# Performance work log

Measured on AMD Instinct MI355X. Metric: run time of the kernel, lower is better.

The kernel has to match this reference:

```python
import jax, jax.numpy as jnp
from jax import lax
import numpy as np

COMMITMENT_COST = 0.25
DATA_VARIANCE = 1.0
DN = ('NCHW', 'OIHW', 'NCHW')


def _conv(x, w, b, stride, pad):
    y = lax.conv_general_dilated(x, w, (stride, stride), ((pad, pad), (pad, pad)), dimension_numbers=DN)
    return y + b[None, :, None, None]


def _conv_t(x, w, b, stride, pad, out_pad):
    # PyTorch ConvTranspose2d(w: [Cin, Cout, kH, kW]) == dilated conv with flipped, transposed kernel
    wf = jnp.flip(w, (2, 3)).transpose(1, 0, 2, 3)  # -> [Cout, Cin, kH, kW]
    k = w.shape[2]
    lo, hi = k - 1 - pad, k - 1 - pad + out_pad
    y = lax.conv_general_dilated(x, wf, (1, 1), ((lo, hi), (lo, hi)), lhs_dilation=(stride, stride), dimension_numbers=DN)
    return y + b[None, :, None, None]


def setup_inputs() -> dict:
    key = jax.random.key(0)
    ks = jax.random.split(key, 14)
    n = lambda k, shp, s: (jax.random.normal(k, shp, dtype=jnp.float32) * s)
    return {
        'x': n(ks[0], (64, 3, 256, 256), 1.0),
        'enc_w1': n(ks[1], (32, 3, 3, 3), 0.2), 'enc_b1': n(ks[2], (32,), 0.02),
        'enc_w2': n(ks[3], (64, 32, 3, 3), 0.06), 'enc_b2': n(ks[4], (64,), 0.02),
        'enc_w3': n(ks[5], (16, 64, 1, 1), 0.12), 'enc_b3': n(ks[6], (16,), 0.02),
        'codebook': n(ks[7], (512, 16), 1.0),
        'dec_w1': n(ks[8], (16, 64, 3, 3), 0.08), 'dec_b1': n(ks[9], (64,), 0.02),
        'dec_w2': n(ks[10], (64, 32, 3, 3), 0.04), 'dec_b2': n(ks[11], (32,), 0.02),
        'dec_w3': n(ks[12], (32, 3, 3, 3), 0.06), 'dec_b3': n(ks[13], (3,), 0.02),
    }


def reference(x, enc_w1, enc_b1, enc_w2, enc_b2, enc_w3, enc_b3, codebook,
              dec_w1, dec_b1, dec_w2, dec_b2, dec_w3, dec_b3):
    # Encoder: 3 -> 32 (s2) -> 64 (s2) -> D (1x1)
    z = jax.nn.relu(_conv(x, enc_w1, enc_b1, 2, 1))
    z = jax.nn.relu(_conv(z, enc_w2, enc_b2, 2, 1))
    z = _conv(z, enc_w3, enc_b3, 1, 0)  # [B, D, H/4, W/4]

    # Vector quantization (training path)
    zp = z.transpose(0, 2, 3, 1)                      # [B, h, w, D]
    D = zp.shape[-1]
    flat = zp.reshape(-1, D)                          # [N, D]
    dist = (jnp.sum(flat * flat, axis=1, keepdims=True)
            + jnp.sum(codebook * codebook, axis=1)
            - 2.0 * flat @ codebook.T)                # [N, K]
    idx = jnp.argmin(dist, axis=1)                    # [N]
    quantized = codebook[idx].reshape(zp.shape)       # [B, h, w, D]

    q_latent_loss = jnp.mean((quantized - lax.stop_gradient(zp)) ** 2)
    e_latent_loss = jnp.mean((zp - lax.stop_gradient(quantized)) ** 2)
    e_q_loss = q_latent_loss + COMMITMENT_COST * e_latent_loss

    ste = zp + lax.stop_gradient(quantized - zp)      # straight-through
    e = ste.transpose(0, 3, 1, 2)                     # [B, D, h, w]

    # Decoder: D -> 64 (x2) -> 32 (x2) -> 3
    y = jax.nn.relu(_conv_t(e, dec_w1, dec_b1, 2, 1, 1))
    y = jax.nn.relu(_conv_t(y, dec_w2, dec_b2, 2, 1, 1))
    x_recon = _conv_t(y, dec_w3, dec_b3, 1, 1, 0)

    recon_mse = jnp.mean((x_recon - x) ** 2)
    recon_loss = recon_mse / DATA_VARIANCE
    return jnp.stack([e_q_loss, recon_loss, recon_mse])
```

## Files before the change

kernel.cpp:

```cpp
#include <hip/hip_runtime.h>
#include <hip/hip_bf16.h>


typedef __attribute__((ext_vector_type(8))) short bf16x8;
typedef __attribute__((ext_vector_type(4))) float f32x4;
typedef unsigned short ushort_t;

__device__ __forceinline__ ushort_t f2bf(float v) {
    __hip_bfloat16 h = __float2bfloat16(v);
    return *(ushort_t*)&h;
}
__device__ __forceinline__ float bf2f(ushort_t u) {
    __hip_bfloat16 h = *(__hip_bfloat16*)&u;
    return __bfloat162float(h);
}
__device__ __forceinline__ unsigned pack2r(float a, float b) {
    return (unsigned)f2bf(fmaxf(a, 0.f)) | ((unsigned)f2bf(fmaxf(b, 0.f)) << 16);
}


__global__ void zero_k(float* __restrict__ acc) {
    acc[blockIdx.x * 256 + threadIdx.x] = 0.f;
}

__global__ __launch_bounds__(256) void prep_k(
        const float* __restrict__ ew1, const float* __restrict__ ew2,
        const float* __restrict__ dw1, const float* __restrict__ dw2,
        const float* __restrict__ dw3, const float* __restrict__ cb,
        ushort_t* __restrict__ wt, float* __restrict__ cn) {
    int idx = blockIdx.x * 256 + threadIdx.x;
    if (idx < 1024) {
        int co = idx >> 5, k = idx & 31;
        wt[idx] = (k < 27) ? f2bf(ew1[co * 27 + k]) : (ushort_t)0;
    } else if (idx < 19456) {
        int i = idx - 1024;
        int t = i >> 11, co = (i >> 5) & 63, ci = i & 31;
        int lci = ((ci & 1) << 4) | (ci >> 1);
        wt[idx] = f2bf(ew2[co * 288 + lci * 9 + t]);
    } else if (idx < 37888) {
        int i = idx - 19456;
        int t = i >> 11, co = (i >> 5) & 63, k = i & 31;
        wt[idx] = (k < 16) ? f2bf(dw1[k * 576 + co * 9 + t]) : (ushort_t)0;
    } else if (idx < 56320) {
        int i = idx - 37888;
        int t = i >> 11, kc = (i >> 10) & 1, co = (i >> 5) & 31, ci = i & 31;
        int m = kc * 32 + ci;
        int lci = ((m & 3) << 4) | (m >> 2);
        wt[idx] = f2bf(dw2[lci * 288 + co * 9 + t]);
    } else if (idx < 60928) {
        int i = idx - 56320;
        int t = i >> 9, co = (i >> 5) & 15, ci = i & 31;
        int lci = ((ci & 1) << 4) | (ci >> 1);
        wt[idx] = (co < 3) ? f2bf(dw3[lci * 27 + co * 9 + (8 - t)]) : (ushort_t)0;
    } else if (idx < 61440) {
        int k = idx - 60928;
        float s = 0.f;
        #pragma unroll
        for (int d = 0; d < 16; ++d) { float v = cb[k * 16 + d]; s += v * v; }
        cn[k] = s;
    }
}

__global__ __launch_bounds__(256) void pad_k(ushort_t* __restrict__ d1p) {
    const int img = blockIdx.x, tid = threadIdx.x;
    const uint4 z = (uint4){0, 0, 0, 0};
    uint4* b1 = (uint4*)(d1p + (size_t)img * 1065024);
    for (int i = tid; i < 1032; i += 256) b1[132096 + i] = z;
    for (int i = tid; i < 1024; i += 256) {
        int r = i >> 3, u = i & 7;
        b1[(r * 129 + 128) * 8 + u] = z;
    }
}

__global__ __launch_bounds__(256, 4) void conv1_k(const float* __restrict__ x,
        const ushort_t* __restrict__ wt, const float* __restrict__ bias,
        ushort_t* __restrict__ a1) {
    const int by = blockIdx.y, b = by >> 7, oh = by & 127;
    const int tid = threadIdx.x;
    __shared__ __align__(16) ushort_t sX[9 * 264];
    __shared__ int sOff[32];
    for (int i = tid; i < 9 * 264 / 2; i += 256) ((unsigned*)sX)[i] = 0u;
    if (tid < 32) {
        int k = tid, off = 0;
        if (k < 27) { int ci = k / 9, r9 = k % 9, kh = r9 / 3, kw = r9 % 3;
                      off = (ci * 3 + kh) * 264 + kw; }
        sOff[tid] = off;
    }
    __syncthreads();
    #pragma unroll
    for (int it = 0; it < 9; ++it) {
        int slot = it * 256 + tid;
        int ci = slot / 768, r = slot % 768, kh = r >> 8, iw = r & 255;
        int ih = 2 * oh + kh - 1;
        float v = ((unsigned)ih < 256u) ? x[(long)(b * 3 + ci) * 65536 + ih * 256 + iw] : 0.f;
        sX[(ci * 3 + kh) * 264 + iw + 1] = f2bf(v);
    }
    __syncthreads();
    const int lane = tid & 63, wave = tid >> 6, q = lane >> 4, n16 = lane & 15;
    bf16x8 Bw[2];
    #pragma unroll
    for (int u = 0; u < 2; ++u)
        Bw[u] = *(const bf16x8*)(wt + (u * 16 + n16) * 32 + q * 8);
    f32x4 acc[2][2];
    #pragma unroll
    for (int u = 0; u < 2; ++u) {
        float bz = bias[u * 16 + n16];
        acc[0][u] = (f32x4){bz, bz, bz, bz};
        acc[1][u] = (f32x4){bz, bz, bz, bz};
    }
    #pragma unroll
    for (int mf = 0; mf < 2; ++mf) {
        const int m2 = 2 * (wave * 32 + mf * 16 + n16);
        ushort_t av[8];
        #pragma unroll
        for (int j = 0; j < 8; ++j) {
            int k = q * 8 + j;
            av[j] = (k < 27) ? sX[sOff[k] + m2] : (ushort_t)0;
        }
        bf16x8 A = *(bf16x8*)av;
        #pragma unroll
        for (int u = 0; u < 2; ++u)
            acc[mf][u] = __builtin_amdgcn_mfma_f32_16x16x32_bf16(A, Bw[u], acc[mf][u], 0, 0, 0);
    }
    #pragma unroll
    for (int mf = 0; mf < 2; ++mf)
        #pragma unroll
        for (int r = 0; r < 4; ++r) {
            int ow = wave * 32 + mf * 16 + q * 4 + r;
            *(unsigned*)(a1 + ((long)(b * 128 + oh) * 128 + ow) * 32 + n16 * 2) =
                pack2r(acc[mf][0][r], acc[mf][1][r]);
        }
}

__global__ __launch_bounds__(256, 4) void conv2_k(const ushort_t* __restrict__ a1,
        const ushort_t* __restrict__ wt, const float* __restrict__ bias,
        ushort_t* __restrict__ a2) {
    const int by = blockIdx.y, b = by >> 6, oh = by & 63;
    const int tid = threadIdx.x;
    __shared__ __align__(16) ushort_t sA[3 * 2 * 66 * 40];
    uint4* z4 = (uint4*)sA;
    #pragma unroll
    for (int it = 0; it < 8; ++it) {
        int slot = it * 256 + tid;
        if (slot < 1980) z4[slot] = (uint4){0, 0, 0, 0};
    }
    __syncthreads();
    #pragma unroll
    for (int it = 0; it < 6; ++it) {
        int slot = it * 256 + tid;
        if (slot < 1536) {
            int kh = slot >> 9, rem = slot & 511, iw = rem >> 2, ci8 = (rem & 3) << 3;
            int ih = 2 * oh + kh - 1;
            if ((unsigned)ih < 128u) {
                uint4 v = *(const uint4*)(a1 + ((long)(b * 128 + ih) * 128 + iw) * 32 + ci8);
                int idx = iw + 2, p = idx & 1, c = idx >> 1;
                *(uint4*)&sA[((kh * 2 + p) * 66 + c) * 40 + ci8] = v;
            }
        }
    }
    __syncthreads();
    const int lane = tid & 63, wave = tid >> 6, q = lane >> 4, n16 = lane & 15;
    f32x4 acc[4];
    #pragma unroll
    for (int u = 0; u < 4; ++u) {
        float bz = bias[u * 16 + n16];
        acc[u] = (f32x4){bz, bz, bz, bz};
    }
    const int ow = wave * 16 + n16;
    #pragma unroll
    for (int t = 0; t < 9; ++t) {
        const int kh = t / 3, kw = t % 3;
        const int p = (kw == 1) ? 0 : 1;
        const int c = (kw == 0) ? ow : ow + 1;
        bf16x8 A = *(bf16x8*)&sA[((kh * 2 + p) * 66 + c) * 40 + q * 8];
        #pragma unroll
        for (int u = 0; u < 4; ++u) {
            bf16x8 B = *(const bf16x8*)(wt + 1024 + t * 2048 + (u * 16 + n16) * 32 + q * 8);
            acc[u] = __builtin_amdgcn_mfma_f32_16x16x32_bf16(A, B, acc[u], 0, 0, 0);
        }
    }
    #pragma unroll
    for (int r = 0; r < 4; ++r) {
        int owo = wave * 16 + q * 4 + r;
        uint2 pk;
        pk.x = pack2r(acc[0][r], acc[1][r]);
        pk.y = pack2r(acc[2][r], acc[3][r]);
        *(uint2*)(a2 + ((long)(b * 64 + oh) * 64 + owo) * 64 + n16 * 4) = pk;
    }
}

__global__ __launch_bounds__(256) void conv3_vq_k(const ushort_t* __restrict__ a2,
        const float* __restrict__ w3, const float* __restrict__ b3,
        const float* __restrict__ cb, const float* __restrict__ cn,
        ushort_t* __restrict__ e, float* __restrict__ acc) {
    const int base = blockIdx.x * 512 + threadIdx.x;
    __shared__ float sred[4];
    float z[2][16];
    #pragma unroll
    for (int p = 0; p < 2; ++p)
        #pragma unroll
        for (int d = 0; d < 16; ++d) z[p][d] = b3[d];
    #pragma unroll
    for (int p = 0; p < 2; ++p) {
        const ushort_t* arow = a2 + (long)(base + p * 256) * 64;
        #pragma unroll
        for (int c8 = 0; c8 < 8; ++c8) {
            uint4 raw = *(const uint4*)(arow + c8 * 8);
            ushort_t us[8];
            *(uint4*)us = raw;
            #pragma unroll
            for (int j = 0; j < 8; ++j) {
                int m = c8 * 8 + j;
                int lci = ((m & 3) << 4) | (m >> 2);
                float a = bf2f(us[j]);
                #pragma unroll
                for (int d = 0; d < 16; ++d)
                    z[p][d] = fmaf(a, w3[d * 64 + lci], z[p][d]);
            }
        }
    }
    const float4* cb4 = (const float4*)cb;
    float best0 = 1e30f, best1 = 1e30f; int bi0 = 0, bi1 = 0;
    for (int k = 0; k < 512; ++k) {
        float4 c0 = cb4[k * 4 + 0], c1 = cb4[k * 4 + 1];
        float4 c2 = cb4[k * 4 + 2], c3 = cb4[k * 4 + 3];
        float nk = cn[k];
        float d0 = z[0][0]*c0.x + z[0][1]*c0.y + z[0][2]*c0.z + z[0][3]*c0.w
                 + z[0][4]*c1.x + z[0][5]*c1.y + z[0][6]*c1.z + z[0][7]*c1.w
                 + z[0][8]*c2.x + z[0][9]*c2.y + z[0][10]*c2.z + z[0][11]*c2.w
                 + z[0][12]*c3.x + z[0][13]*c3.y + z[0][14]*c3.z + z[0][15]*c3.w;
        float d1 = z[1][0]*c0.x + z[1][1]*c0.y + z[1][2]*c0.z + z[1][3]*c0.w
                 + z[1][4]*c1.x + z[1][5]*c1.y + z[1][6]*c1.z + z[1][7]*c1.w
                 + z[1][8]*c2.x + z[1][9]*c2.y + z[1][10]*c2.z + z[1][11]*c2.w
                 + z[1][12]*c3.x + z[1][13]*c3.y + z[1][14]*c3.z + z[1][15]*c3.w;
        float dist0 = nk - 2.f * d0, dist1 = nk - 2.f * d1;
        if (dist0 < best0) { best0 = dist0; bi0 = k; }
        if (dist1 < best1) { best1 = dist1; bi1 = k; }
    }
    float lsum = 0.f;
    #pragma unroll
    for (int d = 0; d < 16; ++d) {
        float q0 = cb[bi0 * 16 + d], q1 = cb[bi1 * 16 + d];
        float f0 = q0 - z[0][d], f1 = q1 - z[1][d];
        lsum += f0 * f0 + f1 * f1;
        e[(long)base * 16 + d] = f2bf(q0);
        e[(long)(base + 256) * 16 + d] = f2bf(q1);
    }
    #pragma unroll
    for (int off = 32; off > 0; off >>= 1) lsum += __shfl_down(lsum, off, 64);
    if ((threadIdx.x & 63) == 0) sred[threadIdx.x >> 6] = lsum;
    __syncthreads();
    if (threadIdx.x == 0)
        atomicAdd(&acc[(blockIdx.x & 63) << 5],
                  sred[0] + sred[1] + sred[2] + sred[3]);
}

__global__ __launch_bounds__(256, 4) void dec1_k(const ushort_t* __restrict__ e,
        const ushort_t* __restrict__ wt, const float* __restrict__ bias,
        ushort_t* __restrict__ d1p) {
    const int by = blockIdx.y, b = by >> 6, i = by & 63;
    const int tid = threadIdx.x;
    __shared__ __align__(16) ushort_t sE[2 * 66 * 24];
    uint4* z4 = (uint4*)sE;
    #pragma unroll
    for (int it = 0; it < 2; ++it) {
        int slot = it * 256 + tid;
        if (slot < 396) z4[slot] = (uint4){0, 0, 0, 0};
    }
    __syncthreads();
    {
        int dh = tid >> 7, rem = tid & 127, j = rem >> 1, ci8 = (rem & 1) * 8;
        if (i + dh < 64) {
            uint4 v = *(const uint4*)(e + ((long)((b * 64 + i + dh) * 64 + j)) * 16 + ci8);
            *(uint4*)&sE[(dh * 66 + j) * 24 + ci8] = v;
        }
    }
    __syncthreads();
    const int lane = tid & 63, wave = tid >> 6, q = lane >> 4, n16 = lane & 15;
    f32x4 acc[4][4];
    #pragma unroll
    for (int u = 0; u < 4; ++u) {
        float bz = bias[u * 16 + n16];
        #pragma unroll
        for (int c = 0; c < 4; ++c) acc[c][u] = (f32x4){bz, bz, bz, bz};
    }
    const int jl = wave * 16 + n16;
    #pragma unroll
    for (int t = 0; t < 9; ++t) {
        const int kh = t / 3, kw = t % 3;
        const int dh = (kh == 0) ? 1 : 0, dw = (kw == 0) ? 1 : 0;
        const int cls = ((kh != 1) ? 2 : 0) | ((kw != 1) ? 1 : 0);
        bf16x8 A = *(bf16x8*)&sE[(dh * 66 + jl + dw) * 24 + (q & 1) * 8];
        #pragma unroll
        for (int u = 0; u < 4; ++u) {
            bf16x8 B = *(const bf16x8*)(wt + 19456 + t * 2048 + (u * 16 + n16) * 32 + q * 8);
            acc[cls][u] = __builtin_amdgcn_mfma_f32_16x16x32_bf16(A, B, acc[cls][u], 0, 0, 0);
        }
    }
    #pragma unroll
    for (int ph = 0; ph < 2; ++ph)
        #pragma unroll
        for (int pw = 0; pw < 2; ++pw)
            #pragma unroll
            for (int r = 0; r < 4; ++r) {
                int oh = 2 * i + ph;
                int ow = 2 * (wave * 16 + q * 4 + r) + pw;
                uint2 pk;
                pk.x = pack2r(acc[ph * 2 + pw][0][r], acc[ph * 2 + pw][1][r]);
                pk.y = pack2r(acc[ph * 2 + pw][2][r], acc[ph * 2 + pw][3][r]);
                *(uint2*)(d1p + (size_t)b * 1065024 + ((long)oh * 129 + ow) * 64 + n16 * 4) = pk;
            }
}

__global__ __launch_bounds__(256, 3) void dec23_k(const ushort_t* __restrict__ d1p,
        const ushort_t* __restrict__ wt, const float* __restrict__ db2,
        const float* __restrict__ db3, const float* __restrict__ x,
        float* __restrict__ acc) {
    const int bx = blockIdx.x, by = blockIdx.y;
    const int b = by >> 6, i4 = by & 63;
    const int j0 = bx << 7;
    const int tid = threadIdx.x;
    const int lane = tid & 63, wave = tid >> 6, q = lane >> 4, n16 = lane & 15;

    __shared__ __align__(16) ushort_t sT[6 * 132 * 32];
    __shared__ float sred[4];
    uint4* z4 = (uint4*)sT;
    #pragma unroll
    for (int it = 0; it < 13; ++it) {
        int s = it * 256 + tid;
        if (s < 3168) z4[s] = (uint4){0, 0, 0, 0};
    }
    __syncthreads();

    const int bb0 = (j0 >> 1) - 1;
    const ushort_t* dbase = d1p + (size_t)b * 1065024;
    for (int s = 0; s < 3; ++s) {
        const int aidx = (wave + s) & 3;
        const int a = 2 * i4 + aidx - 1;
        const int bt0 = s * 2;
        f32x4 acc2[4][2][2];
        #pragma unroll
        for (int u = 0; u < 2; ++u) {
            float bz = db2[u * 16 + n16];
            #pragma unroll
            for (int c = 0; c < 4; ++c) {
                acc2[c][u][0] = (f32x4){bz, bz, bz, bz};
                acc2[c][u][1] = (f32x4){bz, bz, bz, bz};
            }
        }
        const bool skip0 = (aidx == 0);
        const bool skip1 = (aidx == 3);
        #pragma unroll
        for (int kc = 0; kc < 2; ++kc) {
            bf16x8 A[2][2][2];
            #pragma unroll
            for (int dh = 0; dh < 2; ++dh) {
                int row = a + dh;
                bool rok = (unsigned)row <= 128u;
                int rowc = rok ? row : 0;
                #pragma unroll
                for (int dw = 0; dw < 2; ++dw) {
                    #pragma unroll
                    for (int c = 0; c < 2; ++c) {
                        int col = bb0 + (bt0 + c) * 16 + n16 + dw;
                        bool cok = (unsigned)col <= 128u;
                        int colc = cok ? col : 0;
                        bf16x8 v = *(const bf16x8*)(dbase + ((long)rowc * 129 + colc) * 64 + kc * 32 + q * 8);
                        if (!(rok && cok)) v = (bf16x8){0, 0, 0, 0, 0, 0, 0, 0};
                        A[dh][dw][c] = v;
                    }
                }
            }
#define MF23(cls, kh, kw, dh, dw)                                                   \
            _Pragma("unroll")                                                       \
            for (int u = 0; u < 2; ++u) {                                           \
                bf16x8 Bf = *(const bf16x8*)(wt + 37888 + ((kh) * 3 + (kw)) * 2048  \
                                 + kc * 1024 + (u * 16 + n16) * 32 + q * 8);        \
                acc2[cls][u][0] = __builtin_amdgcn_mfma_f32_16x16x32_bf16(          \
                    A[dh][dw][0], Bf, acc2[cls][u][0], 0, 0, 0);                    \
                acc2[cls][u][1] = __builtin_amdgcn_mfma_f32_16x16x32_bf16(          \
                    A[dh][dw][1], Bf, acc2[cls][u][1], 0, 0, 0);                    \
            }
            if (!skip0) {
                MF23(0, 1, 1, 0, 0)
                MF23(1, 1, 0, 0, 1)  MF23(1, 1, 2, 0, 0)
            }
            if (!skip1) {
                MF23(2, 0, 1, 1, 0)  MF23(2, 2, 1, 0, 0)
                MF23(3, 0, 0, 1, 1)  MF23(3, 0, 2, 1, 0)  MF23(3, 2, 0, 0, 1)  MF23(3, 2, 2, 0, 0)
            }
#undef MF23
        }
        #pragma unroll
        for (int cls = 0; cls < 4; ++cls) {
            int ph = cls >> 1, pw = cls & 1;
            if ((ph == 0 && skip0) || (ph == 1 && skip1)) continue;
            int R = 2 * a + ph;
            if ((unsigned)R >= 256u) continue;
            int Rp = R - 4 * i4 + 1;
            #pragma unroll
            for (int c = 0; c < 2; ++c) {
                #pragma unroll
                for (int r = 0; r < 4; ++r) {
                    int cg = 2 * (bb0 + (bt0 + c) * 16 + q * 4 + r) + pw;
                    int cp = 2 * ((bt0 + c) * 16 + q * 4 + r) + pw - 1;
                    if ((unsigned)cg < 256u && (unsigned)cp < 130u) {
                        *(unsigned*)&sT[Rp * 4224 + cp * 32 + n16 * 2] =
                            pack2r(acc2[cls][0][c][r], acc2[cls][1][c][r]);
                    }
                }
            }
        }
    }
    __syncthreads();

    bf16x8 Bw[9];
    #pragma unroll
    for (int t = 0; t < 9; ++t)
        Bw[t] = *(const bf16x8*)(wt + 56320 + t * 512 + n16 * 32 + q * 8);
    float bz3 = (n16 < 3) ? db3[n16] : 0.f;
    f32x4 a4[8];
    #pragma unroll
    for (int mf = 0; mf < 8; ++mf) a4[mf] = (f32x4){bz3, bz3, bz3, bz3};
    const int oh = 4 * i4 + wave;
    #pragma unroll
    for (int kh = 0; kh < 3; ++kh) {
        const ushort_t* srow = &sT[(wave + kh) * 4224];
        #pragma unroll
        for (int mf = 0; mf < 8; ++mf) {
            #pragma unroll
            for (int kw = 0; kw < 3; ++kw) {
                bf16x8 A = *(const bf16x8*)(srow + (mf * 16 + n16 + kw) * 32 + q * 8);
                a4[mf] = __builtin_amdgcn_mfma_f32_16x16x32_bf16(A, Bw[kh * 3 + kw], a4[mf], 0, 0, 0);
            }
        }
    }
    float lsum = 0.f;
    if (n16 < 3) {
        const float* xrow = x + ((long)(b * 3 + n16) * 256 + oh) * 256 + j0;
        #pragma unroll
        for (int mf = 0; mf < 8; ++mf)
            #pragma unroll
            for (int r = 0; r < 4; ++r) {
                int ow = mf * 16 + q * 4 + r;
                float df = a4[mf][r] - xrow[ow];
                lsum += df * df;
            }
    }
    #pragma unroll
    for (int off = 32; off > 0; off >>= 1) lsum += __shfl_down(lsum, off, 64);
    if (lane == 0) sred[wave] = lsum;
    __syncthreads();
    if (tid == 0)
        atomicAdd(&acc[2048 + ((by & 63) << 5)],
                  sred[0] + sred[1] + sred[2] + sred[3]);
}

__global__ void finalize_k(const float* __restrict__ acc, float* __restrict__ out) {
    int t = threadIdx.x;
    float v = acc[t << 5];
    float m = acc[2048 + (t << 5)];
    #pragma unroll
    for (int off = 32; off > 0; off >>= 1) {
        v += __shfl_down(v, off, 64);
        m += __shfl_down(m, off, 64);
    }
    if (t == 0) {
        float eq  = 1.25f * v / 4194304.f;
        float mse = m / 12582912.f;
        out[0] = eq;
        out[1] = mse;
        out[2] = mse;
    }
}

extern "C" void kernel_launch(void* const* d_in, const int* in_sizes, int n_in,
                              void* d_out, int out_size, void* d_ws, size_t ws_size,
                              hipStream_t stream) {
    (void)in_sizes; (void)n_in; (void)out_size;
    const float* x   = (const float*)d_in[0];
    const float* ew1 = (const float*)d_in[1];
    const float* eb1 = (const float*)d_in[2];
    const float* ew2 = (const float*)d_in[3];
    const float* eb2 = (const float*)d_in[4];
    const float* ew3 = (const float*)d_in[5];
    const float* eb3 = (const float*)d_in[6];
    const float* cb  = (const float*)d_in[7];
    const float* dw1 = (const float*)d_in[8];
    const float* db1 = (const float*)d_in[9];
    const float* dw2 = (const float*)d_in[10];
    const float* db2 = (const float*)d_in[11];
    const float* dw3 = (const float*)d_in[12];
    const float* db3 = (const float*)d_in[13];
    float* out = (float*)d_out;

    int C = 64;
    while (C > 1 && (size_t)147456 + (size_t)C * 2261120UL > ws_size) C >>= 1;

    char* base = (char*)d_ws;
    float*    acc = (float*)base;
    ushort_t* wt  = (ushort_t*)(base + 16384);
    float*    cn  = (float*)(base + 16384 + 121856);
    ushort_t* e   = (ushort_t*)(base + 147456);
    char*     rgn = base + 147456 + (size_t)C * 131072UL;
    ushort_t* a1  = (ushort_t*)rgn;
    ushort_t* a2  = (ushort_t*)(rgn + (size_t)C * 1048576UL);
    ushort_t* d1p = (ushort_t*)rgn;

    zero_k<<<16, 256, 0, stream>>>(acc);
    prep_k<<<240, 256, 0, stream>>>(ew1, ew2, dw1, dw2, dw3, cb, wt, cn);

    for (int b0 = 0; b0 < 64; b0 += C) {
        const float* xc = x + (size_t)b0 * 196608UL;
        conv1_k   <<<dim3(1, C * 128), 256, 0, stream>>>(xc,  wt, eb1, a1);
        conv2_k   <<<dim3(1, C * 64),  256, 0, stream>>>(a1,  wt, eb2, a2);
        conv3_vq_k<<<dim3(C * 8),      256, 0, stream>>>(a2,  ew3, eb3, cb, cn, e, acc);
        pad_k     <<<dim3(C),          256, 0, stream>>>(d1p);
        dec1_k    <<<dim3(1, C * 64),  256, 0, stream>>>(e,   wt, db1, d1p);
        dec23_k   <<<dim3(2, C * 64),  256, 0, stream>>>(d1p, wt, db2, db3, xc, acc);
    }
    finalize_k<<<1, 64, 0, stream>>>(acc, out);
}
```

Before: 736.3 us.

## Restructure decoder layer-2 transposed conv to per-wave row with phase-serial accumulation

Replaces the 3-step rotating loop, where each wave handled two column tiles per step and kept accumulators for all four output phases, with one fixed input row per wave. Each wave now covers all five column tiles and processes the output phases one after another, reusing one set of five accumulator pairs. Row and column offsets are precomputed and clamped instead of masked with zeros. The intent is to cut loop and indexing overhead and register pressure and to improve load reuse. The trade-off is that B weight fragments are reloaded for each tap and the A loads are repeated per phase.

```diff
diff --git a/kernel.cpp b/kernel.cpp
--- a/kernel.cpp
+++ b/kernel.cpp
@@ -334,84 +334,80 @@
 
     const int bb0 = (j0 >> 1) - 1;
     const ushort_t* dbase = d1p + (size_t)b * 1065024;
-    for (int s = 0; s < 3; ++s) {
-        const int aidx = (wave + s) & 3;
-        const int a = 2 * i4 + aidx - 1;
-        const int bt0 = s * 2;
-        f32x4 acc2[4][2][2];
-        #pragma unroll
-        for (int u = 0; u < 2; ++u) {
-            float bz = db2[u * 16 + n16];
-            #pragma unroll
-            for (int c = 0; c < 4; ++c) {
-                acc2[c][u][0] = (f32x4){bz, bz, bz, bz};
-                acc2[c][u][1] = (f32x4){bz, bz, bz, bz};
-            }
-        }
-        const bool skip0 = (aidx == 0);
-        const bool skip1 = (aidx == 3);
-        #pragma unroll
-        for (int kc = 0; kc < 2; ++kc) {
-            bf16x8 A[2][2][2];
-            #pragma unroll
-            for (int dh = 0; dh < 2; ++dh) {
-                int row = a + dh;
-                bool rok = (unsigned)row <= 128u;
-                int rowc = rok ? row : 0;
-                #pragma unroll
-                for (int dw = 0; dw < 2; ++dw) {
-                    #pragma unroll
-                    for (int c = 0; c < 2; ++c) {
-                        int col = bb0 + (bt0 + c) * 16 + n16 + dw;
-                        bool cok = (unsigned)col <= 128u;
-                        int colc = cok ? col : 0;
-                        bf16x8 v = *(const bf16x8*)(dbase + ((long)rowc * 129 + colc) * 64 + kc * 32 + q * 8);
-                        if (!(rok && cok)) v = (bf16x8){0, 0, 0, 0, 0, 0, 0, 0};
-                        A[dh][dw][c] = v;
-                    }
-                }
-            }
-#define MF23(cls, kh, kw, dh, dw)                                                   \
+    const int aidx = wave;
+    const int a = 2 * i4 + aidx - 1;
+    const bool doP0 = (aidx != 0);
+    const bool doP1 = (aidx != 3);
+    int r0 = a, r1 = a + 1;
+    r0 = ((unsigned)r0 <= 128u) ? r0 : 128;
+    r1 = ((unsigned)r1 <= 128u) ? r1 : 128;
+    const ushort_t* rowp0 = dbase + (long)r0 * 8256;
+    const ushort_t* rowp1 = dbase + (long)r1 * 8256;
+    int colo[5][2];
+    #pragma unroll
+    for (int cell = 0; cell < 5; ++cell)
+        #pragma unroll
+        for (int dw = 0; dw < 2; ++dw) {
+            int col = bb0 + cell * 16 + n16 + dw;
+            colo[cell][dw] = (((unsigned)col <= 128u) ? col : 128) * 64;
+        }
+    const float bz0 = db2[n16], bz1 = db2[16 + n16];
+    f32x4 a5[2][5];
+
+#define INIT5()                                                                     \
+    _Pragma("unroll")                                                               \
+    for (int cell = 0; cell < 5; ++cell) {                                          \
+        a5[0][cell] = (f32x4){bz0, bz0, bz0, bz0};                                  \
+        a5[1][cell] = (f32x4){bz1, bz1, bz1, bz1};                                  \
+    }
+#define TAP5(T, DH, DW)                                                             \
+    {                                                                               \
+        const ushort_t* wb = wt + 37888 + (T) * 2048;                               \
+        const ushort_t* rp = (DH) ? rowp1 : rowp0;                                  \
+        _Pragma("unroll")                                                           \
+        for (int kc = 0; kc < 2; ++kc) {                                            \
+            bf16x8 B0 = *(const bf16x8*)(wb + kc * 1024 + n16 * 32 + q * 8);        \
+            bf16x8 B1 = *(const bf16x8*)(wb + kc * 1024 + (16 + n16) * 32 + q * 8); \
             _Pragma("unroll")                                                       \
-            for (int u = 0; u < 2; ++u) {                                           \
-                bf16x8 Bf = *(const bf16x8*)(wt + 37888 + ((kh) * 3 + (kw)) * 2048  \
-                                 + kc * 1024 + (u * 16 + n16) * 32 + q * 8);        \
-                acc2[cls][u][0] = __builtin_amdgcn_mfma_f32_16x16x32_bf16(          \
-                    A[dh][dw][0], Bf, acc2[cls][u][0], 0, 0, 0);                    \
-                acc2[cls][u][1] = __builtin_amdgcn_mfma_f32_16x16x32_bf16(          \
-                    A[dh][dw][1], Bf, acc2[cls][u][1], 0, 0, 0);                    \
-            }
-            if (!skip0) {
-                MF23(0, 1, 1, 0, 0)
-                MF23(1, 1, 0, 0, 1)  MF23(1, 1, 2, 0, 0)
-            }
-            if (!skip1) {
-                MF23(2, 0, 1, 1, 0)  MF23(2, 2, 1, 0, 0)
-                MF23(3, 0, 0, 1, 1)  MF23(3, 0, 2, 1, 0)  MF23(3, 2, 0, 0, 1)  MF23(3, 2, 2, 0, 0)
-            }
-#undef MF23
-        }
-        #pragma unroll
-        for (int cls = 0; cls < 4; ++cls) {
-            int ph = cls >> 1, pw = cls & 1;
-            if ((ph == 0 && skip0) || (ph == 1 && skip1)) continue;
-            int R = 2 * a + ph;
-            if ((unsigned)R >= 256u) continue;
-            int Rp = R - 4 * i4 + 1;
-            #pragma unroll
-            for (int c = 0; c < 2; ++c) {
-                #pragma unroll
-                for (int r = 0; r < 4; ++r) {
-                    int cg = 2 * (bb0 + (bt0 + c) * 16 + q * 4 + r) + pw;
-                    int cp = 2 * ((bt0 + c) * 16 + q * 4 + r) + pw - 1;
-                    if ((unsigned)cg < 256u && (unsigned)cp < 130u) {
-                        *(unsigned*)&sT[Rp * 4224 + cp * 32 + n16 * 2] =
-                            pack2r(acc2[cls][0][c][r], acc2[cls][1][c][r]);
-                    }
-                }
-            }
-        }
-    }
+            for (int cell = 0; cell < 5; ++cell) {                                  \
+                bf16x8 Av = *(const bf16x8*)(rp + colo[cell][DW] + kc * 32 + q * 8);\
+                a5[0][cell] = __builtin_amdgcn_mfma_f32_16x16x32_bf16(              \
+                    Av, B0, a5[0][cell], 0, 0, 0);                                  \
+                a5[1][cell] = __builtin_amdgcn_mfma_f32_16x16x32_bf16(              \
+                    Av, B1, a5[1][cell], 0, 0, 0);                                  \
+            }                                                                       \
+        }                                                                           \
+    }
+#define EPI5(PH, PW)                                                                \
+    {                                                                               \
+        int R = 2 * a + (PH);                                                       \
+        if ((unsigned)R < 256u) {                                                   \
+            int Rp = R - 4 * i4 + 1;                                                \
+            _Pragma("unroll")                                                       \
+            for (int cell = 0; cell < 5; ++cell)                                    \
+                _Pragma("unroll")                                                   \
+                for (int r = 0; r < 4; ++r) {                                       \
+                    int lq = cell * 16 + q * 4 + r;                                 \
+                    int cp = 2 * lq + (PW) - 1;                                     \
+                    int cg = 2 * (bb0 + lq) + (PW);                                 \
+                    if ((unsigned)cg < 256u && (unsigned)cp < 130u)                 \
+                        *(unsigned*)&sT[Rp * 4224 + cp * 32 + n16 * 2] =            \
+                            pack2r(a5[0][cell][r], a5[1][cell][r]);                 \
+                }                                                                   \
+        }                                                                           \
+    }
+    if (doP0) {
+        INIT5(); TAP5(4, 0, 0); EPI5(0, 0);
+        INIT5(); TAP5(3, 0, 1); TAP5(5, 0, 0); EPI5(0, 1);
+    }
+    if (doP1) {
+        INIT5(); TAP5(1, 1, 0); TAP5(7, 0, 0); EPI5(1, 0);
+        INIT5(); TAP5(0, 1, 1); TAP5(2, 1, 0); TAP5(6, 0, 1); TAP5(8, 0, 0);
+        EPI5(1, 1);
+    }
+#undef INIT5
+#undef TAP5
+#undef EPI5
     __syncthreads();
 
     bf16x8 Bw[9];
```

Result: faster. 660.4 us (-10.3%).
